# Optimization experiments

Hardware: AMD Instinct MI355X
Metric: run time of the kernel (lower is better)

The kernel has to match this reference:

```python
import jax, jax.numpy as jnp
import numpy as np

B, R, C = 4, 36, 3          # batch, n_rotations, kernel_dim/output_dim
H, W = 384, 224             # padded image spatial: (320+64, 160+64)
CROP = 64
PAD = CROP // 2             # pad_size = 32


def setup_inputs() -> dict:
    key = jax.random.key(0)
    k1, k2 = jax.random.split(key)
    logits = jax.random.normal(k1, (B, C, H, W), dtype=jnp.float32)
    kernel = jax.random.normal(k2, (B * R, C, CROP, CROP), dtype=jnp.float32)
    return {"logits": logits, "kernel": kernel}


def _correlate(logits, kernel):
    # Original computes a full B x (B*R) cross-correlation via F.conv2d and then
    # discards all off-diagonal blocks. A grouped conv (feature_group_count=B)
    # computes exactly the kept diagonal blocks: group i correlates sample i's
    # feature map with that sample's R rotated kernels. interpolate/crop are
    # per-channel/per-pixel so they commute with the channel selection -> same math.
    b, c, h, w = logits.shape
    r = kernel.shape[0] // b
    x = logits.reshape(1, b * c, h, w)
    out = jax.lax.conv_general_dilated(
        x, kernel,
        window_strides=(1, 1),
        padding=[(PAD, PAD), (PAD, PAD)],
        dimension_numbers=("NCHW", "OIHW", "NCHW"),
        feature_group_count=b,
    )  # [1, b*r, h+1, w+1]  (h + 2*PAD - CROP + 1 = h + 1)
    out = out.reshape(b, r, out.shape[-2], out.shape[-1])
    # F.interpolate(..., mode='bilinear', align_corners=False) == half-pixel
    # bilinear resize without antialiasing.
    out = jax.image.resize(out, (b, r, h, w), method="bilinear", antialias=False)
    out = out[:, :, PAD:-PAD, PAD:-PAD]  # [b, r, h-2*PAD, w-2*PAD] = [b, r, 320, 160]
    hc, wc = out.shape[-2], out.shape[-1]
    # softmax over the flattened per-sample (rotation x spatial) map
    flat = jax.nn.softmax(out.reshape(b, -1), axis=-1)
    return flat.reshape(b, r, hc, wc)


def reference(logits, kernel):
    return _correlate(logits, kernel)
```

## Files before the change

### kernel.cpp

```cpp
#include <hip/hip_runtime.h>

typedef short bf16x8 __attribute__((ext_vector_type(8)));
typedef float f32x4  __attribute__((ext_vector_type(4)));
typedef unsigned short u16;

#define B_ 4
#define R_ 36
#define RP 48
#define C_ 3
#define H_ 384
#define W_ 224
#define KS 64
#define OY 321
#define OX 161
#define HC 320
#define WC 160
#define LCOLS 128
#define PITCH 120
#define GR 3072
#define BLKS_PER_BATCH 7200

__device__ __forceinline__ u16 bf16rtn(float v) {
    union { float f; unsigned u; } U; U.f = v;
    unsigned r = U.u + 0x7fffu + ((U.u >> 16) & 1u);
    return (u16)(r >> 16);
}
__device__ __forceinline__ float bf16tof(u16 h) {
    union { float f; unsigned u; } U; U.u = ((unsigned)h) << 16; return U.f;
}

__device__ __forceinline__ float wave_max(float v) {
    #pragma unroll
    for (int off = 32; off > 0; off >>= 1) v = fmaxf(v, __shfl_down(v, off, 64));
    return v;
}
__device__ __forceinline__ float wave_sum(float v) {
    #pragma unroll
    for (int off = 32; off > 0; off >>= 1) v += __shfl_down(v, off, 64);
    return v;
}

__device__ __forceinline__ void dma16(const u16* g, u16* l) {
    __builtin_amdgcn_global_load_lds(
        (const __attribute__((address_space(1))) void*)g,
        (__attribute__((address_space(3))) void*)l, 16, 0, 0);
}

__global__ __launch_bounds__(256) void prep_weights(
    const float* __restrict__ wk, u16* __restrict__ wa)
{
    int d = blockIdx.x * 256 + threadIdx.x;
    int ky32  = d & 31;
    int t1    = d >> 5;
    int r     = t1 % 48;
    int t2    = t1 / 48;
    int plane = t2 & 1;
    int g2    = t2 >> 1;
    int kycp  = g2 & 1;
    int kx    = (g2 >> 1) & 63;
    int bc    = g2 >> 7;
    int c     = bc % 3;
    int b     = bc / 3;
    int ky    = kycp*32 + ky32;
    float v = 0.f;
    if (r < R_) v = wk[(((size_t)(b*R_ + r)*C_ + c)*KS + ky)*KS + kx];
    u16 h = bf16rtn(v);
    u16 o = plane ? bf16rtn(v - bf16tof(h)) : h;
    wa[(size_t)g2*GR + plane*1536 + r*32 + (ky32 ^ (((r >> 1) & 3) << 3))] = o;
}

template<int NT>
__device__ __forceinline__ void conv_body(
    const float* __restrict__ in, const u16* __restrict__ wa,
    float* __restrict__ out, u16* Lh, u16* Ll, u16* Ab, int x0, int y0)
{
    const int b    = blockIdx.z;
    const int t    = threadIdx.x;
    const int w    = __builtin_amdgcn_readfirstlane(t >> 6);
    const int lane = t & 63;
    const int nu   = lane & 15;
    const int q    = lane >> 4;

    f32x4 acc[2][3][NT];
    #pragma unroll
    for (int yi = 0; yi < 2; yi++)
        #pragma unroll
        for (int mi = 0; mi < 3; mi++)
            #pragma unroll
            for (int n = 0; n < NT; n++)
                acc[yi][mi][n] = (f32x4){0.f, 0.f, 0.f, 0.f};

    const u16* gbase = wa + (size_t)(b*384)*GR;

    {
        const u16* s0 = gbase + lane*8;
        if (w < 2) { dma16(s0 + (2*w)*512, Ab + (2*w)*512);
                     dma16(s0 + (2*w+1)*512, Ab + (2*w+1)*512); }
        else       { dma16(s0 + (w+2)*512, Ab + (w+2)*512); }
    }

    for (int c = 0; c < C_; c++) {
        __syncthreads();
        const float* src = in + ((size_t)(b*C_ + c))*H_*W_;
        #pragma unroll
        for (int k = 0; k < 8; k++) {
            int idx = t + 256*k;
            if (idx < 1920) {
                int a    = idx & 31;
                int pr   = (idx >> 5) + ((a >> 3) & 3);
                if (pr >= 60) pr -= 60;
                int r0   = pr * 2;
                int c4   = a * 4;
                int gx   = x0 + c4;
                int gy   = y0 + r0;
                float4 va = make_float4(0.f,0.f,0.f,0.f), vb = va;
                if (gx < W_) {
                    if (gy < H_)     va = *(const float4*)(src + (size_t)gy*W_ + gx);
                    if (gy + 1 < H_) vb = *(const float4*)(src + (size_t)(gy+1)*W_ + gx);
                }
                const float* pa = &va.x;
                const float* pb = &vb.x;
                #pragma unroll
                for (int j = 0; j < 4; j++) {
                    int col = c4 + j;
                    u16 ha = bf16rtn(pa[j]);
                    u16 hb = bf16rtn(pb[j]);
                    u16 la = bf16rtn(pa[j] - bf16tof(ha));
                    u16 lb = bf16rtn(pb[j] - bf16tof(hb));
                    *(unsigned*)&Lh[col*PITCH + r0] = (unsigned)ha | ((unsigned)hb << 16);
                    *(unsigned*)&Ll[col*PITCH + r0] = (unsigned)la | ((unsigned)lb << 16);
                }
            }
        }
        __syncthreads();

        #pragma unroll 1
        for (int gi = 0; gi < 128; gi++) {
            const int g = c*128 + gi;
            __builtin_amdgcn_s_waitcnt(0x3F70);
            __builtin_amdgcn_s_barrier();
            if (g + 1 < 384) {
                const u16* s2 = gbase + (size_t)(g+1)*GR + lane*8;
                u16* d2 = Ab + ((g+1) & 1)*GR;
                if (w < 2) { dma16(s2 + (2*w)*512, d2 + (2*w)*512);
                             dma16(s2 + (2*w+1)*512, d2 + (2*w+1)*512); }
                else       { dma16(s2 + (w+2)*512, d2 + (w+2)*512); }
            }
            const u16* Abp = Ab + (g & 1)*GR;
            const int kx   = gi >> 1;
            const int kycp = gi & 1;

            bf16x8 Ah[3], Al[3];
            #pragma unroll
            for (int mi = 0; mi < 3; mi++) {
                int off = (mi*16 + nu)*32 + ((8*q) ^ (((nu >> 1) & 3) << 3));
                Ah[mi] = *(const bf16x8*)(Abp + off);
                Al[mi] = *(const bf16x8*)(Abp + 1536 + off);
            }
            const u16* colbase = Lh + (size_t)(nu + kx)*PITCH + 32*kycp + 8*q + 8*w;
            #pragma unroll
            for (int n = 0; n < NT; n++) {
                #pragma unroll
                for (int yi = 0; yi < 2; yi++) {
                    const u16* ph = colbase + n*16*PITCH + 32*yi;
                    bf16x8 Bh = *(const bf16x8*)ph;
                    bf16x8 Bl = *(const bf16x8*)(ph + (size_t)LCOLS*PITCH);
                    #pragma unroll
                    for (int mi = 0; mi < 3; mi++) {
                        acc[yi][mi][n] = __builtin_amdgcn_mfma_f32_16x16x32_bf16(Ah[mi], Bh, acc[yi][mi][n], 0, 0, 0);
                        acc[yi][mi][n] = __builtin_amdgcn_mfma_f32_16x16x32_bf16(Ah[mi], Bl, acc[yi][mi][n], 0, 0, 0);
                        acc[yi][mi][n] = __builtin_amdgcn_mfma_f32_16x16x32_bf16(Al[mi], Bh, acc[yi][mi][n], 0, 0, 0);
                    }
                }
            }
        }
    }

    #pragma unroll
    for (int yi = 0; yi < 2; yi++) {
        const int y = y0 + 8*w + 32*yi;
        if (y <= 320) {
            #pragma unroll
            for (int mi = 0; mi < 3; mi++) {
                #pragma unroll
                for (int n = 0; n < NT; n++) {
                    #pragma unroll
                    for (int i = 0; i < 4; i++) {
                        int r = mi*16 + q*4 + i;
                        int x = x0 + n*16 + nu;
                        if (r < R_ && x < OX)
                            out[((size_t)(b*R_ + r)*OY + y)*OX + x] = acc[yi][mi][n][i];
                    }
                }
            }
        }
    }
}

__global__ __launch_bounds__(256) void conv_mfma(
    const float* __restrict__ in, const u16* __restrict__ wa, float* __restrict__ out)
{
    __shared__ __align__(16) u16 smem[2*LCOLS*PITCH + 2*GR];
    u16* Lh = smem;
    u16* Ll = smem + LCOLS*PITCH;
    u16* Ab = smem + 2*LCOLS*PITCH;
    const int s  = blockIdx.y;
    const int y0 = (s < 40) ? ((s >> 3)*64 + (s & 7)) : 320;

    if (blockIdx.x == 0)      conv_body<4>(in, wa, out, Lh, Ll, Ab, 0,   y0);
    else if (blockIdx.x == 1) conv_body<4>(in, wa, out, Lh, Ll, Ab, 64,  y0);
    else                      conv_body<3>(in, wa, out, Lh, Ll, Ab, 128, y0);
}

__global__ __launch_bounds__(256) void resize_kernel(
    const float* __restrict__ cv, float* __restrict__ out, float* __restrict__ pmax)
{
    const int t = threadIdx.x;
    const int idx = blockIdx.x * 256 + t;
    const int j = idx % WC;
    const int rest = idx / WC;
    const int i = rest % HC;
    const int br = rest / HC;

    float fy = (i + 32.5f) * (1.0f/384.0f);
    float fx = (j + 32.5f) * (1.0f/224.0f);

    const float* p = cv + ((size_t)br*OY + i)*OX + j;
    float v00 = p[0], v01 = p[1], v10 = p[OX], v11 = p[OX+1];
    float v = (1.f-fy)*((1.f-fx)*v00 + fx*v01) + fy*((1.f-fx)*v10 + fx*v11);
    out[idx] = v;

    __shared__ float sm[4];
    float m = wave_max(v);
    if ((t & 63) == 0) sm[t >> 6] = m;
    __syncthreads();
    if (t == 0) pmax[blockIdx.x] = fmaxf(fmaxf(sm[0], sm[1]), fmaxf(sm[2], sm[3]));
}

__global__ __launch_bounds__(256) void reduce_kernel(
    const float* __restrict__ part, float* __restrict__ res, int n, int is_sum)
{
    const int b = blockIdx.x;
    const int t = threadIdx.x;
    const float* p = part + (size_t)b*n;
    float v = is_sum ? 0.f : -3.0e38f;
    for (int k = t; k < n; k += 256) v = is_sum ? (v + p[k]) : fmaxf(v, p[k]);
    __shared__ float sm[4];
    float w = is_sum ? wave_sum(v) : wave_max(v);
    if ((t & 63) == 0) sm[t >> 6] = w;
    __syncthreads();
    if (t == 0) {
        res[b] = is_sum ? (sm[0]+sm[1]+sm[2]+sm[3])
                        : fmaxf(fmaxf(sm[0], sm[1]), fmaxf(sm[2], sm[3]));
    }
}

__global__ __launch_bounds__(256) void exp_kernel(
    float* __restrict__ out, const float* __restrict__ bmax, float* __restrict__ psum)
{
    const int t = threadIdx.x;
    const int idx = blockIdx.x * 256 + t;
    const int b = blockIdx.x / BLKS_PER_BATCH;
    float e = expf(out[idx] - bmax[b]);
    out[idx] = e;
    __shared__ float sm[4];
    float s = wave_sum(e);
    if ((t & 63) == 0) sm[t >> 6] = s;
    __syncthreads();
    if (t == 0) psum[blockIdx.x] = sm[0]+sm[1]+sm[2]+sm[3];
}

__global__ __launch_bounds__(256) void scale_kernel(
    float* __restrict__ out, const float* __restrict__ bsum)
{
    const int idx = blockIdx.x * 256 + threadIdx.x;
    const int b = blockIdx.x / BLKS_PER_BATCH;
    out[idx] = out[idx] / bsum[b];
}

extern "C" void kernel_launch(void* const* d_in, const int* in_sizes, int n_in,
                              void* d_out, int out_size, void* d_ws, size_t ws_size,
                              hipStream_t stream)
{
    const float* logits = (const float*)d_in[0];
    const float* wk     = (const float*)d_in[1];
    float* out = (float*)d_out;
    char*  wsB = (char*)d_ws;

    float* convOut = (float*)wsB;
    u16*   wa      = (u16*)(wsB + 29768256);
    float* pmax    = (float*)(wsB + 29768256 + 9437184);
    float* psum    = pmax + 28800;
    float* bmax    = psum + 28800;
    float* bsum    = bmax + 8;

    hipLaunchKernelGGL(prep_weights, dim3(18432), dim3(256), 0, stream, wk, wa);
    hipLaunchKernelGGL(conv_mfma,    dim3(3, 41, B_), dim3(256), 0, stream, logits, wa, convOut);
    hipLaunchKernelGGL(resize_kernel, dim3(28800), dim3(256), 0, stream, convOut, out, pmax);
    hipLaunchKernelGGL(reduce_kernel, dim3(4),     dim3(256), 0, stream, pmax, bmax, BLKS_PER_BATCH, 0);
    hipLaunchKernelGGL(exp_kernel,    dim3(28800), dim3(256), 0, stream, out, bmax, psum);
    hipLaunchKernelGGL(reduce_kernel, dim3(4),     dim3(256), 0, stream, psum, bsum, BLKS_PER_BATCH, 1);
    hipLaunchKernelGGL(scale_kernel,  dim3(28800), dim3(256), 0, stream, out, bsum);
}
```

Baseline: 670.9 us.

## Load weight fragments directly into registers with register double-buffering

Replaces the LDS double-buffered weight staging, filled by global_load_lds DMA with a per-step waitcnt and block barrier, with direct per-wave global loads of the A fragments into registers. The next kx/ky step is prefetched into a second register set while MFMAs run on the current one, and the loop is unrolled by two to ping-pong the sets. This drops a barrier per inner step and shrinks LDS use, which may allow more resident blocks. The cost is that every wave now loads the same weights redundantly from global memory or L2, and register pressure goes up.

Result: no change. 662.4 us (-1.3%).

```diff
diff --git a/kernel.cpp b/kernel.cpp
--- a/kernel.cpp
+++ b/kernel.cpp
@@ -38,12 +38,6 @@
     #pragma unroll
     for (int off = 32; off > 0; off >>= 1) v += __shfl_down(v, off, 64);
     return v;
-}
-
-__device__ __forceinline__ void dma16(const u16* g, u16* l) {
-    __builtin_amdgcn_global_load_lds(
-        (const __attribute__((address_space(1))) void*)g,
-        (__attribute__((address_space(3))) void*)l, 16, 0, 0);
 }
 
 __global__ __launch_bounds__(256) void prep_weights(
@@ -72,7 +66,7 @@
 template<int NT>
 __device__ __forceinline__ void conv_body(
     const float* __restrict__ in, const u16* __restrict__ wa,
-    float* __restrict__ out, u16* Lh, u16* Ll, u16* Ab, int x0, int y0)
+    float* __restrict__ out, u16* Lh, u16* Ll, int x0, int y0)
 {
     const int b    = blockIdx.z;
     const int t    = threadIdx.x;
@@ -92,12 +86,44 @@
 
     const u16* gbase = wa + (size_t)(b*384)*GR;
 
-    {
-        const u16* s0 = gbase + lane*8;
-        if (w < 2) { dma16(s0 + (2*w)*512, Ab + (2*w)*512);
-                     dma16(s0 + (2*w+1)*512, Ab + (2*w+1)*512); }
-        else       { dma16(s0 + (w+2)*512, Ab + (w+2)*512); }
-    }
+    const int sw   = (8*q) ^ (((nu >> 1) & 3) << 3);
+    const int offH = nu*32 + sw;
+
+    bf16x8 A0h[3], A0l[3], A1h[3], A1l[3];
+
+    #pragma unroll
+    for (int mi = 0; mi < 3; mi++) {
+        A0h[mi] = *(const bf16x8*)(gbase + offH + mi*512);
+        A0l[mi] = *(const bf16x8*)(gbase + 1536 + offH + mi*512);
+    }
+
+#define STEP(G, CH, CL, NH, NL) do {                                         \
+    int gn_ = (G) + 1; if (gn_ > 383) gn_ = 383;                             \
+    const u16* gp_ = gbase + (size_t)gn_ * GR;                               \
+    _Pragma("unroll")                                                        \
+    for (int mi = 0; mi < 3; mi++) {                                         \
+        NH[mi] = *(const bf16x8*)(gp_ + offH + mi*512);                      \
+        NL[mi] = *(const bf16x8*)(gp_ + 1536 + offH + mi*512);               \
+    }                                                                        \
+    const int kx_   = ((G) & 127) >> 1;                                      \
+    const int kycp_ = (G) & 1;                                               \
+    const u16* cb_ = Lh + (size_t)(nu + kx_)*PITCH + 32*kycp_ + 8*q + 8*w;   \
+    _Pragma("unroll")                                                        \
+    for (int n = 0; n < NT; n++) {                                           \
+        _Pragma("unroll")                                                    \
+        for (int yi = 0; yi < 2; yi++) {                                     \
+            const u16* ph_ = cb_ + n*16*PITCH + 32*yi;                       \
+            bf16x8 Bh_ = *(const bf16x8*)ph_;                                \
+            bf16x8 Bl_ = *(const bf16x8*)(ph_ + (size_t)LCOLS*PITCH);        \
+            _Pragma("unroll")                                                \
+            for (int mi = 0; mi < 3; mi++) {                                 \
+                acc[yi][mi][n] = __builtin_amdgcn_mfma_f32_16x16x32_bf16(CH[mi], Bh_, acc[yi][mi][n], 0, 0, 0); \
+                acc[yi][mi][n] = __builtin_amdgcn_mfma_f32_16x16x32_bf16(CH[mi], Bl_, acc[yi][mi][n], 0, 0, 0); \
+                acc[yi][mi][n] = __builtin_amdgcn_mfma_f32_16x16x32_bf16(CL[mi], Bh_, acc[yi][mi][n], 0, 0, 0); \
+            }                                                                \
+        }                                                                    \
+    }                                                                        \
+} while (0)
 
     for (int c = 0; c < C_; c++) {
         __syncthreads();
@@ -135,46 +161,13 @@
         __syncthreads();
 
         #pragma unroll 1
-        for (int gi = 0; gi < 128; gi++) {
-            const int g = c*128 + gi;
-            __builtin_amdgcn_s_waitcnt(0x3F70);
-            __builtin_amdgcn_s_barrier();
-            if (g + 1 < 384) {
-                const u16* s2 = gbase + (size_t)(g+1)*GR + lane*8;
-                u16* d2 = Ab + ((g+1) & 1)*GR;
-                if (w < 2) { dma16(s2 + (2*w)*512, d2 + (2*w)*512);
-                             dma16(s2 + (2*w+1)*512, d2 + (2*w+1)*512); }
-                else       { dma16(s2 + (w+2)*512, d2 + (w+2)*512); }
-            }
-            const u16* Abp = Ab + (g & 1)*GR;
-            const int kx   = gi >> 1;
-            const int kycp = gi & 1;
-
-            bf16x8 Ah[3], Al[3];
-            #pragma unroll
-            for (int mi = 0; mi < 3; mi++) {
-                int off = (mi*16 + nu)*32 + ((8*q) ^ (((nu >> 1) & 3) << 3));
-                Ah[mi] = *(const bf16x8*)(Abp + off);
-                Al[mi] = *(const bf16x8*)(Abp + 1536 + off);
-            }
-            const u16* colbase = Lh + (size_t)(nu + kx)*PITCH + 32*kycp + 8*q + 8*w;
-            #pragma unroll
-            for (int n = 0; n < NT; n++) {
-                #pragma unroll
-                for (int yi = 0; yi < 2; yi++) {
-                    const u16* ph = colbase + n*16*PITCH + 32*yi;
-                    bf16x8 Bh = *(const bf16x8*)ph;
-                    bf16x8 Bl = *(const bf16x8*)(ph + (size_t)LCOLS*PITCH);
-                    #pragma unroll
-                    for (int mi = 0; mi < 3; mi++) {
-                        acc[yi][mi][n] = __builtin_amdgcn_mfma_f32_16x16x32_bf16(Ah[mi], Bh, acc[yi][mi][n], 0, 0, 0);
-                        acc[yi][mi][n] = __builtin_amdgcn_mfma_f32_16x16x32_bf16(Ah[mi], Bl, acc[yi][mi][n], 0, 0, 0);
-                        acc[yi][mi][n] = __builtin_amdgcn_mfma_f32_16x16x32_bf16(Al[mi], Bh, acc[yi][mi][n], 0, 0, 0);
-                    }
-                }
-            }
+        for (int gi2 = 0; gi2 < 128; gi2 += 2) {
+            const int g = c*128 + gi2;
+            STEP(g,     A0h, A0l, A1h, A1l);
+            STEP(g + 1, A1h, A1l, A0h, A0l);
         }
     }
+#undef STEP
 
     #pragma unroll
     for (int yi = 0; yi < 2; yi++) {
@@ -200,16 +193,15 @@
 __global__ __launch_bounds__(256) void conv_mfma(
     const float* __restrict__ in, const u16* __restrict__ wa, float* __restrict__ out)
 {
-    __shared__ __align__(16) u16 smem[2*LCOLS*PITCH + 2*GR];
+    __shared__ __align__(16) u16 smem[2*LCOLS*PITCH];
     u16* Lh = smem;
     u16* Ll = smem + LCOLS*PITCH;
-    u16* Ab = smem + 2*LCOLS*PITCH;
     const int s  = blockIdx.y;
     const int y0 = (s < 40) ? ((s >> 3)*64 + (s & 7)) : 320;
 
-    if (blockIdx.x == 0)      conv_body<4>(in, wa, out, Lh, Ll, Ab, 0,   y0);
-    else if (blockIdx.x == 1) conv_body<4>(in, wa, out, Lh, Ll, Ab, 64,  y0);
-    else                      conv_body<3>(in, wa, out, Lh, Ll, Ab, 128, y0);
+    if (blockIdx.x == 0)      conv_body<4>(in, wa, out, Lh, Ll, 0,   y0);
+    else if (blockIdx.x == 1) conv_body<4>(in, wa, out, Lh, Ll, 64,  y0);
+    else                      conv_body<3>(in, wa, out, Lh, Ll, 128, y0);
 }
 
 __global__ __launch_bounds__(256) void resize_kernel(
```
